# Kernel tuning notes

Hardware: AMD Instinct MI355X
Metric: run time of the kernel (lower is better)

## Reference

```python
import jax, jax.numpy as jnp
import numpy as np

# static config (matches init_kwargs)
B, T, D = 4, 1024, 512
H, G = 8, 2
HD = D // H            # 64
REP = H // G           # 4
CHUNK = 64
LC = 2 * CHUNK         # left_context = context_chunk_number * chunk_size = 128
MAXPOS = CHUNK + LC    # 192
NLAYER = 4
EPS = 1e-4
NEG = -50000.0


def _ln(x, w, b):
    m = x.mean(-1, keepdims=True)
    v = ((x - m) ** 2).mean(-1, keepdims=True)
    return (x - m) / jnp.sqrt(v + EPS) * w + b


def _chunk_mask(mask_length):
    # get_mask_vector(CHUNK, mask_length, LC)
    corr = (mask_length + CHUNK - 1) // CHUNK * CHUNK
    row = jnp.arange(corr)[:, None]
    col = jnp.arange(corr + LC)[None, :]
    start = (row // CHUNK) * CHUNK
    cm = (col >= start) & (col < start + CHUNK + LC)
    cm = cm[:mask_length, LC:LC + mask_length]
    return jnp.where(cm, 0.0, -jnp.inf)


def _cut_masks(mask, lens):
    # _cut_masks_with_len_vector
    Lm = mask.shape[0]
    lim = (lens + LC)[:, None]                      # [B,1]
    inb = jnp.arange(Lm)[None, :] < lim             # [B,Lm]
    valid = inb[:, :, None] & inb[:, None, :]       # [B,Lm,Lm]
    return jnp.where(valid, mask[None], NEG)


def _attn(xp, wq, wk, wv, wo, rel_tab, mask):
    # GQASelfAttentionRelPos forward. xp:[B,Tp,D], mask:[B,Tp,Tp]
    Bb, Tp, _ = xp.shape
    scale = 1.0 / jnp.sqrt(jnp.float32(HD))
    q = (xp @ wq.T).reshape(Bb, Tp, H, HD) * scale
    k = jnp.repeat((xp @ wk.T).reshape(Bb, Tp, G, HD), REP, axis=2)
    v = jnp.repeat((xp @ wv.T).reshape(Bb, Tp, G, HD), REP, axis=2)
    scores = jnp.einsum('bqhd,bkhd->bhqk', q, k)
    r = jnp.arange(Tp)
    dist = jnp.clip(r[None, :] - r[:, None], -(MAXPOS - 1), MAXPOS - 1) + MAXPOS - 1
    rel = rel_tab[dist]                              # [Tp,Tp,HD], row=query
    scores = scores + jnp.einsum('bqhd,kqd->bhqk', q, rel)  # matches 'bhd,thd->bht'
    scores = scores + mask[:, None]                  # broadcast over heads
    p = jax.nn.softmax(scores, axis=-1)
    out = jnp.einsum('bhqk,bkhd->bqhd', p, v).reshape(Bb, Tp, D)
    return out @ wo.T


def _conv(x, pw1, dw, pw2):
    # Conformer-style ConvModule(d_model, kernel=9): pointwise->GLU->depthwise->SiLU->pointwise
    h = x @ pw1.T                                   # [B,T,2D]
    a, g = jnp.split(h, 2, axis=-1)
    h = a * jax.nn.sigmoid(g)                       # GLU
    h = jnp.transpose(h, (0, 2, 1))                 # [B,D,T]
    h = jax.lax.conv_general_dilated(h, dw[:, None, :], (1,), [(4, 4)],
                                     dimension_numbers=('NCH', 'OIH', 'NCH'),
                                     feature_group_count=D)
    h = jax.nn.silu(h)
    h = jnp.transpose(h, (0, 2, 1))
    return h @ pw2.T


def _ffn(x, w1, w2):
    # SwiGLUFFN(factor=2)
    h = x @ w1.T
    a, b = jnp.split(h, 2, axis=-1)
    return (jax.nn.silu(a) * b) @ w2.T


def setup_inputs() -> dict:
    key = jax.random.key(0)
    ks = iter(jax.random.split(key, 40))
    s = 0.02
    def rn(shape):
        return jax.random.normal(next(ks), shape, jnp.float32) * s
    L = NLAYER
    return {
        'x': jax.random.normal(next(ks), (B, T, D), jnp.float32),
        'audio_len': jax.random.randint(next(ks), (B,), 1, T + 1),
        'ln1_w': jnp.ones((L, D), jnp.float32), 'ln1_b': jnp.zeros((L, D), jnp.float32),
        'wq': rn((L, D, D)), 'wk': rn((L, G * HD, D)), 'wv': rn((L, G * HD, D)), 'wo': rn((L, D, D)),
        'rel_emb': rn((L, 2 * MAXPOS - 1, HD)),
        'ln2_w': jnp.ones((L, D), jnp.float32), 'ln2_b': jnp.zeros((L, D), jnp.float32),
        'conv_pw1': rn((L, 2 * D, D)), 'conv_dw': rn((L, D, 9)), 'conv_pw2': rn((L, D, D)),
        'ln3_w': jnp.ones((L, D), jnp.float32), 'ln3_b': jnp.zeros((L, D), jnp.float32),
        'ffn_w1': rn((L, 4 * D, D)), 'ffn_w2': rn((L, D, 2 * D)),
    }


def reference(x, audio_len, ln1_w, ln1_b, wq, wk, wv, wo, rel_emb,
              ln2_w, ln2_b, conv_pw1, conv_dw, conv_pw2,
              ln3_w, ln3_b, ffn_w1, ffn_w2):
    mask = _cut_masks(_chunk_mask(T + LC), audio_len)   # [B,Tp,Tp]
    for i in range(NLAYER):
        x = _ln(x, ln1_w[i], ln1_b[i])
        xp = jnp.pad(x, ((0, 0), (LC, 0), (0, 0)))
        x = x + _attn(xp, wq[i], wk[i], wv[i], wo[i], rel_emb[i], mask)[:, LC:]
        x = _ln(x, ln2_w[i], ln2_b[i])
        x = x + _conv(x, conv_pw1[i], conv_dw[i], conv_pw2[i])
        x = _ln(x, ln3_w[i], ln3_b[i])
        x = x + _ffn(x, ffn_w1[i], ffn_w2[i])
    return x
```

## Files before the change

kernel.cpp:

```cpp
#include <hip/hip_runtime.h>
#include <hip/hip_bf16.h>

typedef __hip_bfloat16 bf16;
typedef unsigned short ushort_t;
typedef unsigned int uint_t;
typedef __attribute__((ext_vector_type(8))) short short8;
typedef __attribute__((ext_vector_type(4))) float floatx4;

__device__ __forceinline__ float b2f(bf16 x) { return __bfloat162float(x); }
__device__ __forceinline__ ushort_t f2us(float f) { bf16 h = __float2bfloat16(f); return *(ushort_t*)&h; }
__device__ __forceinline__ float us2f(ushort_t u) { return __uint_as_float(((uint_t)u) << 16); }

constexpr int Bc = 4, Tc = 1024, Dc = 512, Hc = 8, HDc = 64;
constexpr int LCc = 128, MPc = 192;
constexpr float EPSc = 1e-4f;
constexpr int NBT = Bc * Tc;
constexpr long NE = (long)NBT * Dc;
constexpr float NEGB = -1e30f;
constexpr int PSTRIDE = 8704;
constexpr int QSTR = 768;

__device__ __forceinline__ float wload(const void* p, long i, int f32) {
  return f32 ? ((const float*)p)[i] : b2f(((const bf16*)p)[i]);
}

template<int N> __device__ __forceinline__ void vmwait() {
  if constexpr (N == 0)      asm volatile("s_waitcnt vmcnt(0)" ::: "memory");
  else if constexpr (N == 4) asm volatile("s_waitcnt vmcnt(4)" ::: "memory");
  else if constexpr (N == 6) asm volatile("s_waitcnt vmcnt(6)" ::: "memory");
  else if constexpr (N == 8) asm volatile("s_waitcnt vmcnt(8)" ::: "memory");
  else if constexpr (N == 12) asm volatile("s_waitcnt vmcnt(12)" ::: "memory");
  else static_assert(N == 0, "unsupported vmcnt literal");
}

__device__ __forceinline__ void stage_swz(const ushort_t* __restrict__ G, int rowStride,
                                          int rowBase, int k0, ushort_t* L, int nChunk, int t) {
#pragma unroll
  for (int i = t; i < nChunk; i += 256) {
    int r = i >> 3;
    int cs = (i & 7) ^ (r & 7);
    const ushort_t* gp = G + (long)(rowBase + r) * rowStride + k0 + cs * 8;
    __builtin_amdgcn_global_load_lds(
        (const __attribute__((address_space(1))) void*)gp,
        (__attribute__((address_space(3))) void*)&L[(i & ~63) * 8], 16, 0, 0);
  }
}

__global__ void k_detect(const void* __restrict__ x, int* __restrict__ flag) {
  __shared__ int s[256];
  int t = threadIdx.x;
  const unsigned short* u = (const unsigned short*)x;
  int bad = 0;
  for (int j = t; j < 2048; j += 256) {
    int e = (u[j] >> 7) & 0xFF;
    if (e == 0xFF || e > 0x8F || (e != 0 && e < 0x6F)) bad++;
  }
  s[t] = bad;
  __syncthreads();
  for (int off = 128; off > 0; off >>= 1) { if (t < off) s[t] += s[t + off]; __syncthreads(); }
  if (t == 0) flag[0] = (s[0] > 16) ? 1 : 0;
}

__global__ void k_in(const void* __restrict__ in, float* __restrict__ out, int n,
                     const int* __restrict__ flag) {
  int i = blockIdx.x * 256 + threadIdx.x;
  if (i < n) out[i] = wload(in, i, flag[0]);
}
__global__ void k_out(const float* __restrict__ in, void* __restrict__ out, int n,
                      const int* __restrict__ flag) {
  int i = blockIdx.x * 256 + threadIdx.x;
  if (i >= n) return;
  if (flag[0]) ((float*)out)[i] = in[i];
  else         ((bf16*)out)[i] = __float2bfloat16(in[i]);
}

__global__ void k_w2all(const void* wq, const void* wk, const void* wv, const void* wo,
                        const void* rel, const void* pw1, const void* dwv, const void* pw2,
                        const void* w1, const void* w2,
                        ushort_t* __restrict__ wbf, const int* __restrict__ flag) {
  int f32 = flag[0];
  long i = (long)blockIdx.x * 256 + threadIdx.x;
  if (i >= 12175104L) return;
  float v;
  if (i < 1572864) {
    long l = i / 393216, rem = i - l * 393216;
    int r = (int)(rem >> 9), c = (int)(rem & 511);
    if (r < 512)      v = 0.125f * wload(wq, l * 262144 + (long)r * 512 + c, f32);
    else if (r < 640) v = wload(wk, l * 65536 + (long)(r - 512) * 512 + c, f32);
    else              v = wload(wv, l * 65536 + (long)(r - 640) * 512 + c, f32);
  } else if (i < 2621440) {
    v = wload(wo, i - 1572864, f32);
  } else if (i < 2719488) {
    v = wload(rel, i - 2621440, f32);
  } else if (i < 4816640) {
    v = wload(pw1, i - 2719488, f32);
  } else if (i < 4835072) {
    long r2 = i - 4816640;
    long l = r2 / 4608, rem = r2 - l * 4608;
    int j = (int)(rem >> 9), d = (int)(rem & 511);
    v = wload(dwv, l * 4608 + (long)d * 9 + j, f32);
  } else if (i < 5883648) {
    v = wload(pw2, i - 4835072, f32);
  } else if (i < 10077952) {
    v = wload(w1, i - 5883648, f32);
  } else {
    v = wload(w2, i - 10077952, f32);
  }
  wbf[i] = f2us(v);
}

__global__ __launch_bounds__(256) void k_ln(const float* __restrict__ x,
    const void* __restrict__ w, const void* __restrict__ bb, long woff,
    float* __restrict__ o, ushort_t* __restrict__ oA, const int* __restrict__ flag) {
  int f32 = flag[0];
  int row = blockIdx.x;
  int t = threadIdx.x;
  int lane = t & 63, wv = t >> 6;
  float2 v = ((const float2*)(x + (long)row * Dc))[t];
  float s = v.x + v.y;
#pragma unroll
  for (int o2 = 1; o2 < 64; o2 <<= 1) s += __shfl_xor(s, o2, 64);
  __shared__ float ws[8];
  if (lane == 0) ws[wv] = s;
  __syncthreads();
  float mean = (ws[0] + ws[1] + ws[2] + ws[3]) * (1.0f / Dc);
  float dx = v.x - mean, dy = v.y - mean;
  float s2 = dx * dx + dy * dy;
#pragma unroll
  for (int o2 = 1; o2 < 64; o2 <<= 1) s2 += __shfl_xor(s2, o2, 64);
  if (lane == 0) ws[4 + wv] = s2;
  __syncthreads();
  float inv = 1.0f / sqrtf((ws[4] + ws[5] + ws[6] + ws[7]) * (1.0f / Dc) + EPSc);
  float v0 = dx * inv * wload(w, woff + 2 * t, f32)     + wload(bb, woff + 2 * t, f32);
  float v1 = dy * inv * wload(w, woff + 2 * t + 1, f32) + wload(bb, woff + 2 * t + 1, f32);
  float2 ov; ov.x = v0; ov.y = v1;
  ((float2*)(o + (long)row * Dc))[t] = ov;
  ((uint_t*)(oA + (long)row * Dc))[t] = (uint_t)f2us(v0) | ((uint_t)f2us(v1) << 16);
}

template<int BM, int BN, bool OBF>
__global__ __launch_bounds__(256) void k_gemm_b(const ushort_t* __restrict__ A, int lda,
    const ushort_t* __restrict__ W, void* __restrict__ C, int ldc,
    const float* __restrict__ addend, float alpha, int K) {
  constexpr int WGM = BM / 64;
  constexpr int WGN = 4 / WGM;
  constexpr int WN = BN / WGN;
  constexpr int NJ = WN / 16;
  constexpr int LPI = (BM * 8 + BN * 8) / 256;
  __shared__ ushort_t As[2][BM * 64];
  __shared__ ushort_t Ws[2][BN * 64];
  int t = threadIdx.x;
  int m0 = blockIdx.y * BM, n0 = blockIdx.x * BN;
  int lane = t & 63, wv = t >> 6;
  int l15 = lane & 15, quad = lane >> 4;
  int wrow = (WGM == 2) ? (wv >> 1) * 64 : 0;
  int wcol = (WGM == 2) ? (wv & 1) * WN : wv * WN;
  floatx4 acc[4][NJ];
#pragma unroll
  for (int i = 0; i < 4; ++i)
#pragma unroll
    for (int j = 0; j < NJ; ++j) acc[i][j] = 0;
  stage_swz(A, lda, m0, 0, As[0], BM * 8, t);
  stage_swz(W, K,  n0, 0, Ws[0], BN * 8, t);
  int cur = 0;
  for (int k0 = 0; k0 < K; k0 += 64) {
    int nk = k0 + 64;
    if (nk < K) {
      stage_swz(A, lda, m0, nk, As[cur ^ 1], BM * 8, t);
      stage_swz(W, K,  n0, nk, Ws[cur ^ 1], BN * 8, t);
      vmwait<LPI>();
    } else {
      vmwait<0>();
    }
    __builtin_amdgcn_s_barrier();
    __builtin_amdgcn_sched_barrier(0);
    const ushort_t* Asc = As[cur];
    const ushort_t* Wsc = Ws[cur];
#pragma unroll
    for (int half = 0; half < 2; ++half) {
      int sw = ((half * 4 + quad) ^ (l15 & 7)) << 3;
      short8 af[4], bfr[NJ];
#pragma unroll
      for (int i = 0; i < 4; ++i) af[i] = *(short8*)&Asc[(wrow + i * 16 + l15) * 64 + sw];
#pragma unroll
      for (int j = 0; j < NJ; ++j) bfr[j] = *(short8*)&Wsc[(wcol + j * 16 + l15) * 64 + sw];
#pragma unroll
      for (int i = 0; i < 4; ++i)
#pragma unroll
        for (int j = 0; j < NJ; ++j)
          acc[i][j] = __builtin_amdgcn_mfma_f32_16x16x32_bf16(af[i], bfr[j], acc[i][j], 0, 0, 0);
    }
    __builtin_amdgcn_s_barrier();
    cur ^= 1;
  }
#pragma unroll
  for (int i = 0; i < 4; ++i) {
#pragma unroll
    for (int j = 0; j < NJ; ++j) {
#pragma unroll
      for (int rg = 0; rg < 4; ++rg) {
        int m = m0 + wrow + i * 16 + quad * 4 + rg;
        int n = n0 + wcol + j * 16 + l15;
        float v = alpha * acc[i][j][rg];
        if (addend) v += addend[(long)m * ldc + n];
        if (OBF) ((ushort_t*)C)[(long)m * ldc + n] = f2us(v);
        else     ((float*)C)[(long)m * ldc + n] = v;
      }
    }
  }
}

template<int MODE>
__global__ __launch_bounds__(256) void k_gemm_gate(const ushort_t* __restrict__ A, int lda,
    const ushort_t* __restrict__ Wa, const ushort_t* __restrict__ Wg,
    ushort_t* __restrict__ C, int ldc, int K) {
  __shared__ ushort_t As[2][64 * 64];
  __shared__ ushort_t Wsa[2][64 * 64];
  __shared__ ushort_t Wsg[2][64 * 64];
  int t = threadIdx.x;
  int m0 = blockIdx.y * 64, n0 = blockIdx.x * 64;
  int lane = t & 63, wv = t >> 6;
  int l15 = lane & 15, quad = lane >> 4;
  int wcol = wv * 16;
  floatx4 acca[4], accg[4];
#pragma unroll
  for (int i = 0; i < 4; ++i) { acca[i] = 0; accg[i] = 0; }
  stage_swz(A, lda, m0, 0, As[0], 512, t);
  stage_swz(Wa, K, n0, 0, Wsa[0], 512, t);
  stage_swz(Wg, K, n0, 0, Wsg[0], 512, t);
  int cur = 0;
  for (int k0 = 0; k0 < K; k0 += 64) {
    int nk = k0 + 64;
    if (nk < K) {
      stage_swz(A, lda, m0, nk, As[cur ^ 1], 512, t);
      stage_swz(Wa, K, n0, nk, Wsa[cur ^ 1], 512, t);
      stage_swz(Wg, K, n0, nk, Wsg[cur ^ 1], 512, t);
      vmwait<6>();
    } else {
      vmwait<0>();
    }
    __builtin_amdgcn_s_barrier();
    __builtin_amdgcn_sched_barrier(0);
    const ushort_t* Asc = As[cur];
    const ushort_t* Wac = Wsa[cur];
    const ushort_t* Wgc = Wsg[cur];
#pragma unroll
    for (int half = 0; half < 2; ++half) {
      int sw = ((half * 4 + quad) ^ (l15 & 7)) << 3;
      short8 af[4], ba, bg;
#pragma unroll
      for (int i = 0; i < 4; ++i) af[i] = *(short8*)&Asc[(i * 16 + l15) * 64 + sw];
      ba = *(short8*)&Wac[(wcol + l15) * 64 + sw];
      bg = *(short8*)&Wgc[(wcol + l15) * 64 + sw];
#pragma unroll
      for (int i = 0; i < 4; ++i) {
        acca[i] = __builtin_amdgcn_mfma_f32_16x16x32_bf16(af[i], ba, acca[i], 0, 0, 0);
        accg[i] = __builtin_amdgcn_mfma_f32_16x16x32_bf16(af[i], bg, accg[i], 0, 0, 0);
      }
    }
    __builtin_amdgcn_s_barrier();
    cur ^= 1;
  }
#pragma unroll
  for (int i = 0; i < 4; ++i) {
#pragma unroll
    for (int rg = 0; rg < 4; ++rg) {
      int m = m0 + i * 16 + quad * 4 + rg;
      int n = n0 + wcol + l15;
      float a = acca[i][rg], g = accg[i][rg];
      float v;
      if (MODE == 0) v = a * (1.0f / (1.0f + __expf(-g)));
      else           v = (a / (1.0f + __expf(-a))) * g;
      C[(long)m * ldc + n] = f2us(v);
    }
  }
}

__global__ __launch_bounds__(256, 3) void k_attn(const ushort_t* __restrict__ qkv,
    const ushort_t* __restrict__ relL, const int* __restrict__ alen,
    ushort_t* __restrict__ out, char* __restrict__ part) {
  int bx = blockIdx.x;
  int h = blockIdx.y, b = blockIdx.z;
  int len = alen[b];
  int inv, qt, grp;
  if (bx < 16) { inv = 0; qt = bx; grp = 0; }
  else         { inv = 1; qt = (bx - 16) & 15; grp = (bx - 16) >> 4; }
  int q0 = qt * 64;
  if (inv) { if (q0 + 64 <= len) return; }
  else     { if (q0 >= len) return; }
  int nvalid = min(len - q0, 64);
  int g = h >> 2;
  __shared__ __align__(16) ushort_t UQB[8704];
  __shared__ __align__(16) ushort_t Ks[64 * 64];
  __shared__ __align__(16) ushort_t Vt[64 * 72];
  __shared__ __align__(16) ushort_t Ps[64 * 64];
  __shared__ __align__(16) float fML[128];
  ushort_t* Qs = UQB;
  ushort_t* B2t = UQB;
  int t = threadIdx.x;
  int lane = t & 63, w = t >> 6;
  int l15 = lane & 15, quad = lane >> 4;
  int qw = w * 16;
  {
    int qi = t >> 2, du = (t & 3) * 16;
    const ushort_t* src = qkv + ((long)(b * Tc + q0 + qi)) * QSTR + h * 64 + du;
    *(uint4*)&Qs[qi * 72 + du] = *(const uint4*)(src);
    *(uint4*)&Qs[qi * 72 + du + 8] = *(const uint4*)(src + 8);
  }
  const int koB = inv ? -128 : (q0 - 128);
  const int KSTEP = inv ? 4 : 1;
  const int nIt = inv ? ((grp < 2) ? 5 : 4) : 3;
  uint4 kr0, kr1, vr0, vr1;
  int kj = t >> 2, du = (t & 3) * 16, c0 = du >> 3;
  auto LOADKV = [&](int kt2) {
    int ko = koB + kt2 * 64 + kj;
    if (ko >= 0) {
      long basek = ((long)(b * Tc + ko)) * QSTR + 512 + g * 64 + du;
      kr0 = *(const uint4*)(qkv + basek);
      kr1 = *(const uint4*)(qkv + basek + 8);
      vr0 = *(const uint4*)(qkv + basek + 128);
      vr1 = *(const uint4*)(qkv + basek + 136);
    } else {
      uint4 z = {0, 0, 0, 0};
      kr0 = z; kr1 = z; vr0 = z; vr1 = z;
    }
  };
  LOADKV(grp);
  float m_ = NEGB, l_ = 0.f;
  floatx4 acc[4];
#pragma unroll
  for (int j = 0; j < 4; ++j) acc[j] = 0;
  __syncthreads();
  short8 aq0 = *(short8*)&Qs[(qw + l15) * 72 + quad * 8];
  short8 aq1 = *(short8*)&Qs[(qw + l15) * 72 + 32 + quad * 8];
  float rv_lo = 0.f, rv_hi = 0.f;
  if (inv) {
    int er = (l15 == 1) ? 382 : 0;
    short8 be0 = *(const short8*)(relL + (long)er * 64 + quad * 8);
    short8 be1 = *(const short8*)(relL + (long)er * 64 + 32 + quad * 8);
    floatx4 ec = {0.f, 0.f, 0.f, 0.f};
    ec = __builtin_amdgcn_mfma_f32_16x16x32_bf16(be0, aq0, ec, 0, 0, 0);
    ec = __builtin_amdgcn_mfma_f32_16x16x32_bf16(be1, aq1, ec, 0, 0, 0);
    rv_lo = __shfl(ec[0], l15, 64);
    rv_hi = __shfl(ec[1], l15, 64);
  }
  int sw7 = l15 & 7;
  for (int it = 0; it < nIt; ++it) {
    int kt = inv ? (grp + it * KSTEP) : it;
    int ko0 = koB + kt * 64;
    int t0 = q0 - ko0 + 191;
    bool far_hi = (q0 - ko0 - 63) >= 191;
    bool far_lo = (q0 + 63 - ko0) <= -191;
    bool near = !far_hi && !far_lo;
    int cb = min(max(t0 - 63, 0), 255);
    __syncthreads();
    {
      *(uint4*)&Ks[kj * 64 + ((c0 ^ (kj & 7)) << 3)] = kr0;
      *(uint4*)&Ks[kj * 64 + (((c0 + 1) ^ (kj & 7)) << 3)] = kr1;
      uint_t wds[8] = {vr0.x, vr0.y, vr0.z, vr0.w, vr1.x, vr1.y, vr1.z, vr1.w};
#pragma unroll
      for (int u = 0; u < 8; ++u) {
        Vt[(du + 2 * u) * 72 + kj] = (ushort_t)(wds[u] & 0xffff);
        Vt[(du + 2 * u + 1) * 72 + kj] = (ushort_t)(wds[u] >> 16);
      }
    }
    if (near) {
      __builtin_amdgcn_s_setprio(1);
#pragma unroll
      for (int p = 0; p < 2; ++p) {
        short8 rw0[4], rw1[4];
#pragma unroll
        for (int j = 0; j < 4; ++j) {
          long wr = cb + (p * 4 + j) * 16 + l15;
          rw0[j] = *(const short8*)(relL + wr * 64 + quad * 8);
          rw1[j] = *(const short8*)(relL + wr * 64 + 32 + quad * 8);
        }
#pragma unroll
        for (int j = 0; j < 4; ++j) {
          floatx4 z = {0.f, 0.f, 0.f, 0.f};
          z = __builtin_amdgcn_mfma_f32_16x16x32_bf16(rw0[j], aq0, z, 0, 0, 0);
          z = __builtin_amdgcn_mfma_f32_16x16x32_bf16(rw1[j], aq1, z, 0, 0, 0);
#pragma unroll
          for (int rg = 0; rg < 4; ++rg) {
            int cpr = (p * 4 + j) * 16 + quad * 4 + rg;
            B2t[cpr * 68 + qw + l15] = f2us(z[rg]);
          }
        }
      }
      __builtin_amdgcn_s_setprio(0);
    }
    __syncthreads();
    if (it + 1 < nIt) LOADKV(kt + KSTEP);
    floatx4 s[4];
    __builtin_amdgcn_s_setprio(1);
#pragma unroll
    for (int nt = 0; nt < 4; ++nt) {
      short8 ak0 = *(short8*)&Ks[(nt * 16 + l15) * 64 + ((quad ^ sw7) << 3)];
      short8 ak1 = *(short8*)&Ks[(nt * 16 + l15) * 64 + (((4 + quad) ^ sw7) << 3)];
      floatx4 z = {0.f, 0.f, 0.f, 0.f};
      z = __builtin_amdgcn_mfma_f32_16x16x32_bf16(ak0, aq0, z, 0, 0, 0);
      z = __builtin_amdgcn_mfma_f32_16x16x32_bf16(ak1, aq1, z, 0, 0, 0);
      s[nt] = z;
    }
    __builtin_amdgcn_s_setprio(0);
    if (near) {
#pragma unroll
      for (int nt = 0; nt < 4; ++nt)
#pragma unroll
        for (int rg = 0; rg < 4; ++rg) {
          int c = t0 + qw + l15 - (nt * 16 + quad * 4 + rg);
          c = min(max(c, 0), 382);
          s[nt][rg] += us2f(B2t[(c - cb) * 68 + qw + l15]);
        }
    } else {
      float rv = far_hi ? rv_hi : rv_lo;
#pragma unroll
      for (int nt = 0; nt < 4; ++nt)
#pragma unroll
        for (int rg = 0; rg < 4; ++rg) s[nt][rg] += rv;
    }
    if (!inv) {
#pragma unroll
      for (int nt = 0; nt < 4; ++nt)
#pragma unroll
        for (int rg = 0; rg < 4; ++rg) {
          int ko = ko0 + nt * 16 + quad * 4 + rg;
          if (ko >= len) s[nt][rg] = NEGB;
        }
    }
    float mx = s[0][0];
#pragma unroll
    for (int nt = 0; nt < 4; ++nt)
#pragma unroll
      for (int rg = 0; rg < 4; ++rg) mx = fmaxf(mx, s[nt][rg]);
    mx = fmaxf(mx, __shfl_xor(mx, 16, 64));
    mx = fmaxf(mx, __shfl_xor(mx, 32, 64));
    float mn = fmaxf(m_, mx);
    float al = __expf(m_ - mn);
    float ps = 0.f;
#pragma unroll
    for (int nt = 0; nt < 4; ++nt)
#pragma unroll
      for (int rg = 0; rg < 4; ++rg) {
        float p = __expf(s[nt][rg] - mn);
        s[nt][rg] = p;
        ps += p;
      }
    ps += __shfl_xor(ps, 16, 64);
    ps += __shfl_xor(ps, 32, 64);
    l_ = l_ * al + ps;
    m_ = mn;
    if (quad == 0) fML[qw + l15] = al;
#pragma unroll
    for (int nt = 0; nt < 4; ++nt)
#pragma unroll
      for (int pr = 0; pr < 2; ++pr) {
        uint_t pk = (uint_t)f2us(s[nt][2 * pr]) | ((uint_t)f2us(s[nt][2 * pr + 1]) << 16);
        int e = nt * 16 + quad * 4 + pr * 2;
        *(uint_t*)&Ps[(qw + l15) * 64 + (((e >> 3) ^ sw7) << 3) + (e & 7)] = pk;
      }
    floatx4 av = *(floatx4*)&fML[qw + quad * 4];
#pragma unroll
    for (int j = 0; j < 4; ++j)
#pragma unroll
      for (int rg = 0; rg < 4; ++rg) acc[j][rg] *= av[rg];
    short8 ap0 = *(short8*)&Ps[(qw + l15) * 64 + ((quad ^ sw7) << 3)];
    short8 ap1 = *(short8*)&Ps[(qw + l15) * 64 + (((4 + quad) ^ sw7) << 3)];
    __builtin_amdgcn_s_setprio(1);
#pragma unroll
    for (int j = 0; j < 4; ++j) {
      short8 bv0 = *(short8*)&Vt[(j * 16 + l15) * 72 + quad * 8];
      short8 bv1 = *(short8*)&Vt[(j * 16 + l15) * 72 + 32 + quad * 8];
      acc[j] = __builtin_amdgcn_mfma_f32_16x16x32_bf16(ap0, bv0, acc[j], 0, 0, 0);
      acc[j] = __builtin_amdgcn_mfma_f32_16x16x32_bf16(ap1, bv1, acc[j], 0, 0, 0);
    }
    __builtin_amdgcn_s_setprio(0);
  }
  if (inv) {
    char* pp = part + (long)((((b * 8 + h) * 16 + qt) * 4 + grp)) * PSTRIDE;
    ushort_t* Cp = (ushort_t*)pp;
    float* mp = (float*)(pp + 8192);
#pragma unroll
    for (int j = 0; j < 4; ++j)
#pragma unroll
      for (int rg = 0; rg < 4; ++rg)
        Cp[(qw + quad * 4 + rg) * 64 + j * 16 + l15] = f2us(acc[j][rg]);
    if (quad == 0) { mp[qw + l15] = m_; mp[64 + qw + l15] = l_; }
  } else {
    if (quad == 0) fML[64 + qw + l15] = l_;
    floatx4 lv = *(floatx4*)&fML[64 + qw + quad * 4];
#pragma unroll
    for (int rg = 0; rg < 4; ++rg) {
      int R = qw + quad * 4 + rg;
      if (R < nvalid) {
        float invL = 1.0f / lv[rg];
#pragma unroll
        for (int j = 0; j < 4; ++j)
          out[((long)(b * Tc + q0 + R)) * Dc + h * 64 + j * 16 + l15] = f2us(acc[j][rg] * invL);
      }
    }
  }
}

__global__ __launch_bounds__(256) void k_comb(const char* __restrict__ part,
    const int* __restrict__ alen, ushort_t* __restrict__ out) {
  int qt = blockIdx.x, h = blockIdx.y, b = blockIdx.z;
  int len = alen[b];
  int q0 = qt * 64;
  if (q0 + 64 <= len) return;
  int nskip = max(len - q0, 0);
  int t = threadIdx.x;
  int d = t & 63, r0 = (t >> 6) * 16;
  const char* pb = part + (long)(((b * 8 + h) * 16 + qt) * 4) * PSTRIDE;
#pragma unroll 4
  for (int i = 0; i < 16; ++i) {
    int r = r0 + i;
    if (r < nskip) continue;
    float mg[4], lg[4], M = NEGB;
#pragma unroll
    for (int g2 = 0; g2 < 4; ++g2) {
      const float* mp = (const float*)(pb + g2 * PSTRIDE + 8192);
      mg[g2] = mp[r];
      lg[g2] = mp[64 + r];
      M = fmaxf(M, mg[g2]);
    }
    float L = 0.f, wgt[4];
#pragma unroll
    for (int g2 = 0; g2 < 4; ++g2) { wgt[g2] = __expf(mg[g2] - M); L += lg[g2] * wgt[g2]; }
    float v = 0.f;
#pragma unroll
    for (int g2 = 0; g2 < 4; ++g2)
      v += us2f(((const ushort_t*)(pb + g2 * PSTRIDE))[r * 64 + d]) * wgt[g2];
    out[((long)(b * Tc + q0 + r)) * Dc + h * 64 + d] = f2us(v / L);
  }
}

__global__ void k_dwconv(const ushort_t* __restrict__ in, const ushort_t* __restrict__ dwT,
                         ushort_t* __restrict__ out, int n8) {
  int i = blockIdx.x * 256 + threadIdx.x;
  if (i >= n8) return;
  int row = i >> 6;
  int d8 = (i & 63) << 3;
  int t = row & (Tc - 1);
  int b = row >> 10;
  float acc[8] = {0, 0, 0, 0, 0, 0, 0, 0};
#pragma unroll
  for (int j = 0; j < 9; ++j) {
    int tt = t + j - 4;
    if (tt < 0 || tt >= Tc) continue;
    short8 vv = *(const short8*)&in[((long)(b * Tc + tt) << 9) + d8];
    short8 dv = *(const short8*)&dwT[j * 512 + d8];
#pragma unroll
    for (int e = 0; e < 8; ++e)
      acc[e] += us2f((ushort_t)vv[e]) * us2f((ushort_t)dv[e]);
  }
  short8 o8;
#pragma unroll
  for (int e = 0; e < 8; ++e)
    o8[e] = (short)f2us(acc[e] * (1.0f / (1.0f + __expf(-acc[e]))));
  *(short8*)&out[(long)row * 512 + d8] = o8;
}

extern "C" void kernel_launch(void* const* d_in, const int* in_sizes, int n_in,
                              void* d_out, int out_size, void* d_ws, size_t ws_size,
                              hipStream_t stream) {
  const void* x_in = d_in[0];
  const int*  alen = (const int*)d_in[1];
  const void* ln1w = d_in[2];
  const void* ln1b = d_in[3];
  const void* wq   = d_in[4];
  const void* wk   = d_in[5];
  const void* wv   = d_in[6];
  const void* wo   = d_in[7];
  const void* rel  = d_in[8];
  const void* ln2w = d_in[9];
  const void* ln2b = d_in[10];
  const void* pw1  = d_in[11];
  const void* dwv  = d_in[12];
  const void* pw2  = d_in[13];
  const void* ln3w = d_in[14];
  const void* ln3b = d_in[15];
  const void* w1   = d_in[16];
  const void* w2   = d_in[17];

  char* base = (char*)d_ws;
  int*      flag = (int*)base;
  float*    xf   = (float*)(base + 256);
  float*    lnb  = (float*)(base + 256 + 8388608);
  ushort_t* lnA  = (ushort_t*)(base + 16777472);
  ushort_t* wbf  = (ushort_t*)(base + 20971776);
  char*     U    = base + 45321984;
  ushort_t* qkv = (ushort_t*)U;
  ushort_t* ab  = (ushort_t*)(U + 6291456);
  char*     partA = U + 10485760;
  ushort_t* big = (ushort_t*)U;
  ushort_t* cb  = (ushort_t*)(U + 16777216);
  size_t REQ = 45321984 + 16777216 + 4194304;
  size_t REQ2 = 45321984 + 35651584;
  if (REQ2 > REQ) REQ = REQ2;
  if (ws_size < REQ) return;

  ushort_t* qkvB  = wbf + 0;
  ushort_t* woB   = wbf + 1572864;
  ushort_t* relB  = wbf + 2621440;
  ushort_t* pw1B  = wbf + 2719488;
  ushort_t* dwB   = wbf + 4816640;
  ushort_t* pw2B  = wbf + 4835072;
  ushort_t* w1B   = wbf + 5883648;
  ushort_t* w2B   = wbf + 10077952;

  k_detect<<<1, 256, 0, stream>>>(x_in, flag);
  k_in<<<(int)((NE + 255) / 256), 256, 0, stream>>>(x_in, xf, (int)NE, flag);
  k_w2all<<<47559, 256, 0, stream>>>(wq, wk, wv, wo, rel, pw1, dwv, pw2, w1, w2, wbf, flag);

  for (int i = 0; i < 4; ++i) {
    long oLN = (long)i * Dc;
    k_ln<<<NBT, 256, 0, stream>>>(xf, ln1w, ln1b, oLN, lnb, lnA, flag);
    k_gemm_b<64, 64, true><<<dim3(12, 64), 256, 0, stream>>>(lnA, Dc, qkvB + (long)i * 393216, qkv, QSTR, nullptr, 1.0f, 512);
    k_attn<<<dim3(80, 8, 4), 256, 0, stream>>>(qkv, relB + (long)i * 24512, alen, ab, partA);
    k_comb<<<dim3(16, 8, 4), 256, 0, stream>>>(partA, alen, ab);
    k_gemm_b<64, 64, false><<<dim3(8, 64), 256, 0, stream>>>(ab, Dc, woB + (long)i * 262144, xf, Dc, lnb, 1.0f, 512);

    k_ln<<<NBT, 256, 0, stream>>>(xf, ln2w, ln2b, oLN, lnb, lnA, flag);
    k_gemm_gate<0><<<dim3(8, 64), 256, 0, stream>>>(lnA, Dc, pw1B + (long)i * 524288,
        pw1B + (long)i * 524288 + 262144, big, 512, 512);
    k_dwconv<<<NBT * 512 / 8 / 256, 256, 0, stream>>>(big, dwB + (long)i * 4608, cb, NBT * 512 / 8);
    k_gemm_b<64, 64, false><<<dim3(8, 64), 256, 0, stream>>>(cb, Dc, pw2B + (long)i * 262144, xf, Dc, lnb, 1.0f, 512);

    k_ln<<<NBT, 256, 0, stream>>>(xf, ln3w, ln3b, oLN, lnb, lnA, flag);
    k_gemm_gate<1><<<dim3(16, 64), 256, 0, stream>>>(lnA, Dc, w1B + (long)i * 1048576,
        w1B + (long)i * 1048576 + 524288, big, 1024, 512);
    k_gemm_b<64, 64, false><<<dim3(8, 64), 256, 0, stream>>>(big, 1024, w2B + (long)i * 524288, xf, Dc, lnb, 1.0f, 1024);
  }

  k_out<<<(int)((NE + 255) / 256), 256, 0, stream>>>(xf, d_out, (int)NE, flag);
}
```

Before: 833.4 us.

## Write V transposed from QKV GEMM, load Q into registers, warp-per-row LayerNorm

```diff
diff --git a/kernel.cpp b/kernel.cpp
--- a/kernel.cpp
+++ b/kernel.cpp
@@ -29,7 +29,6 @@
   else if constexpr (N == 4) asm volatile("s_waitcnt vmcnt(4)" ::: "memory");
   else if constexpr (N == 6) asm volatile("s_waitcnt vmcnt(6)" ::: "memory");
   else if constexpr (N == 8) asm volatile("s_waitcnt vmcnt(8)" ::: "memory");
-  else if constexpr (N == 12) asm volatile("s_waitcnt vmcnt(12)" ::: "memory");
   else static_assert(N == 0, "unsupported vmcnt literal");
 }
 
@@ -113,35 +112,42 @@
     const void* __restrict__ w, const void* __restrict__ bb, long woff,
     float* __restrict__ o, ushort_t* __restrict__ oA, const int* __restrict__ flag) {
   int f32 = flag[0];
-  int row = blockIdx.x;
   int t = threadIdx.x;
-  int lane = t & 63, wv = t >> 6;
-  float2 v = ((const float2*)(x + (long)row * Dc))[t];
-  float s = v.x + v.y;
+  int lane = t & 63;
+  int row = blockIdx.x * 4 + (t >> 6);
+  const float4* xr = (const float4*)(x + (long)row * Dc);
+  float4 va = xr[lane * 2], vb = xr[lane * 2 + 1];
+  float s = va.x + va.y + va.z + va.w + vb.x + vb.y + vb.z + vb.w;
 #pragma unroll
   for (int o2 = 1; o2 < 64; o2 <<= 1) s += __shfl_xor(s, o2, 64);
-  __shared__ float ws[8];
-  if (lane == 0) ws[wv] = s;
-  __syncthreads();
-  float mean = (ws[0] + ws[1] + ws[2] + ws[3]) * (1.0f / Dc);
-  float dx = v.x - mean, dy = v.y - mean;
-  float s2 = dx * dx + dy * dy;
+  float mean = s * (1.0f / Dc);
+  float d[8] = {va.x - mean, va.y - mean, va.z - mean, va.w - mean,
+                vb.x - mean, vb.y - mean, vb.z - mean, vb.w - mean};
+  float s2 = 0.f;
+#pragma unroll
+  for (int e = 0; e < 8; ++e) s2 += d[e] * d[e];
 #pragma unroll
   for (int o2 = 1; o2 < 64; o2 <<= 1) s2 += __shfl_xor(s2, o2, 64);
-  if (lane == 0) ws[4 + wv] = s2;
-  __syncthreads();
-  float inv = 1.0f / sqrtf((ws[4] + ws[5] + ws[6] + ws[7]) * (1.0f / Dc) + EPSc);
-  float v0 = dx * inv * wload(w, woff + 2 * t, f32)     + wload(bb, woff + 2 * t, f32);
-  float v1 = dy * inv * wload(w, woff + 2 * t + 1, f32) + wload(bb, woff + 2 * t + 1, f32);
-  float2 ov; ov.x = v0; ov.y = v1;
-  ((float2*)(o + (long)row * Dc))[t] = ov;
-  ((uint_t*)(oA + (long)row * Dc))[t] = (uint_t)f2us(v0) | ((uint_t)f2us(v1) << 16);
-}
-
-template<int BM, int BN, bool OBF>
+  float inv = 1.0f / sqrtf(s2 * (1.0f / Dc) + EPSc);
+  float v[8];
+#pragma unroll
+  for (int e = 0; e < 8; ++e)
+    v[e] = d[e] * inv * wload(w, woff + lane * 8 + e, f32) + wload(bb, woff + lane * 8 + e, f32);
+  float4 o0 = {v[0], v[1], v[2], v[3]}, o1 = {v[4], v[5], v[6], v[7]};
+  float4* orow = (float4*)(o + (long)row * Dc);
+  orow[lane * 2] = o0; orow[lane * 2 + 1] = o1;
+  uint4 pk;
+  pk.x = (uint_t)f2us(v[0]) | ((uint_t)f2us(v[1]) << 16);
+  pk.y = (uint_t)f2us(v[2]) | ((uint_t)f2us(v[3]) << 16);
+  pk.z = (uint_t)f2us(v[4]) | ((uint_t)f2us(v[5]) << 16);
+  pk.w = (uint_t)f2us(v[6]) | ((uint_t)f2us(v[7]) << 16);
+  *(uint4*)&oA[(long)row * Dc + lane * 8] = pk;
+}
+
+template<int BM, int BN, bool OBF, int QKV>
 __global__ __launch_bounds__(256) void k_gemm_b(const ushort_t* __restrict__ A, int lda,
     const ushort_t* __restrict__ W, void* __restrict__ C, int ldc,
-    const float* __restrict__ addend, float alpha, int K) {
+    const float* __restrict__ addend, float alpha, int K, ushort_t* __restrict__ vtw) {
   constexpr int WGM = BM / 64;
   constexpr int WGN = 4 / WGM;
   constexpr int WN = BN / WGN;
@@ -193,6 +199,18 @@
     __builtin_amdgcn_s_barrier();
     cur ^= 1;
   }
+  if (QKV && n0 >= 640) {
+#pragma unroll
+    for (int i = 0; i < 4; ++i) {
+      int mb = m0 + i * 16 + quad * 4;
+      int d = n0 - 640 + wcol + l15;
+      uint2 pk;
+      pk.x = (uint_t)f2us(acc[i][0][0]) | ((uint_t)f2us(acc[i][0][1]) << 16);
+      pk.y = (uint_t)f2us(acc[i][0][2]) | ((uint_t)f2us(acc[i][0][3]) << 16);
+      *(uint2*)(vtw + ((long)(mb >> 10)) * 131072 + (long)d * 1024 + (mb & 1023)) = pk;
+    }
+    return;
+  }
 #pragma unroll
   for (int i = 0; i < 4; ++i) {
 #pragma unroll
@@ -277,6 +295,7 @@
 }
 
 __global__ __launch_bounds__(256, 3) void k_attn(const ushort_t* __restrict__ qkv,
+    const ushort_t* __restrict__ vt,
     const ushort_t* __restrict__ relL, const int* __restrict__ alen,
     ushort_t* __restrict__ out, char* __restrict__ part) {
   int bx = blockIdx.x;
@@ -290,36 +309,33 @@
   else     { if (q0 >= len) return; }
   int nvalid = min(len - q0, 64);
   int g = h >> 2;
-  __shared__ __align__(16) ushort_t UQB[8704];
+  __shared__ __align__(16) ushort_t B2t[8704];
   __shared__ __align__(16) ushort_t Ks[64 * 64];
-  __shared__ __align__(16) ushort_t Vt[64 * 72];
+  __shared__ __align__(16) ushort_t Vt[64 * 64];
   __shared__ __align__(16) ushort_t Ps[64 * 64];
   __shared__ __align__(16) float fML[128];
-  ushort_t* Qs = UQB;
-  ushort_t* B2t = UQB;
   int t = threadIdx.x;
   int lane = t & 63, w = t >> 6;
   int l15 = lane & 15, quad = lane >> 4;
   int qw = w * 16;
-  {
-    int qi = t >> 2, du = (t & 3) * 16;
-    const ushort_t* src = qkv + ((long)(b * Tc + q0 + qi)) * QSTR + h * 64 + du;
-    *(uint4*)&Qs[qi * 72 + du] = *(const uint4*)(src);
-    *(uint4*)&Qs[qi * 72 + du + 8] = *(const uint4*)(src + 8);
-  }
+  const ushort_t* qrow = qkv + ((long)(b * Tc + q0 + qw + l15)) * QSTR + h * 64;
+  short8 aq0 = *(const short8*)(qrow + quad * 8);
+  short8 aq1 = *(const short8*)(qrow + 32 + quad * 8);
   const int koB = inv ? -128 : (q0 - 128);
   const int KSTEP = inv ? 4 : 1;
   const int nIt = inv ? ((grp < 2) ? 5 : 4) : 3;
   uint4 kr0, kr1, vr0, vr1;
   int kj = t >> 2, du = (t & 3) * 16, c0 = du >> 3;
+  int vd = t >> 2, vc = (t & 3) * 2;
   auto LOADKV = [&](int kt2) {
-    int ko = koB + kt2 * 64 + kj;
-    if (ko >= 0) {
-      long basek = ((long)(b * Tc + ko)) * QSTR + 512 + g * 64 + du;
+    int ko0x = koB + kt2 * 64;
+    if (ko0x >= 0) {
+      long basek = ((long)(b * Tc + ko0x + kj)) * QSTR + 512 + g * 64 + du;
       kr0 = *(const uint4*)(qkv + basek);
       kr1 = *(const uint4*)(qkv + basek + 8);
-      vr0 = *(const uint4*)(qkv + basek + 128);
-      vr1 = *(const uint4*)(qkv + basek + 136);
+      long basev = (long)b * 131072 + (long)(g * 64 + vd) * 1024 + ko0x + (t & 3) * 16;
+      vr0 = *(const uint4*)(vt + basev);
+      vr1 = *(const uint4*)(vt + basev + 8);
     } else {
       uint4 z = {0, 0, 0, 0};
       kr0 = z; kr1 = z; vr0 = z; vr1 = z;
@@ -330,9 +346,6 @@
   floatx4 acc[4];
 #pragma unroll
   for (int j = 0; j < 4; ++j) acc[j] = 0;
-  __syncthreads();
-  short8 aq0 = *(short8*)&Qs[(qw + l15) * 72 + quad * 8];
-  short8 aq1 = *(short8*)&Qs[(qw + l15) * 72 + 32 + quad * 8];
   float rv_lo = 0.f, rv_hi = 0.f;
   if (inv) {
     int er = (l15 == 1) ? 382 : 0;
@@ -357,12 +370,8 @@
     {
       *(uint4*)&Ks[kj * 64 + ((c0 ^ (kj & 7)) << 3)] = kr0;
       *(uint4*)&Ks[kj * 64 + (((c0 + 1) ^ (kj & 7)) << 3)] = kr1;
-      uint_t wds[8] = {vr0.x, vr0.y, vr0.z, vr0.w, vr1.x, vr1.y, vr1.z, vr1.w};
-#pragma unroll
-      for (int u = 0; u < 8; ++u) {
-        Vt[(du + 2 * u) * 72 + kj] = (ushort_t)(wds[u] & 0xffff);
-        Vt[(du + 2 * u + 1) * 72 + kj] = (ushort_t)(wds[u] >> 16);
-      }
+      *(uint4*)&Vt[vd * 64 + ((vc ^ (vd & 7)) << 3)] = vr0;
+      *(uint4*)&Vt[vd * 64 + (((vc + 1) ^ (vd & 7)) << 3)] = vr1;
     }
     if (near) {
       __builtin_amdgcn_s_setprio(1);
@@ -469,8 +478,9 @@
     __builtin_amdgcn_s_setprio(1);
 #pragma unroll
     for (int j = 0; j < 4; ++j) {
-      short8 bv0 = *(short8*)&Vt[(j * 16 + l15) * 72 + quad * 8];
-      short8 bv1 = *(short8*)&Vt[(j * 16 + l15) * 72 + 32 + quad * 8];
+      int rd = j * 16 + l15;
+      short8 bv0 = *(short8*)&Vt[rd * 64 + ((quad ^ (rd & 7)) << 3)];
+      short8 bv1 = *(short8*)&Vt[rd * 64 + (((4 + quad) ^ (rd & 7)) << 3)];
       acc[j] = __builtin_amdgcn_mfma_f32_16x16x32_bf16(ap0, bv0, acc[j], 0, 0, 0);
       acc[j] = __builtin_amdgcn_mfma_f32_16x16x32_bf16(ap1, bv1, acc[j], 0, 0, 0);
     }
@@ -488,6 +498,7 @@
     if (quad == 0) { mp[qw + l15] = m_; mp[64 + qw + l15] = l_; }
   } else {
     if (quad == 0) fML[64 + qw + l15] = l_;
+    __syncthreads();
     floatx4 lv = *(floatx4*)&fML[64 + qw + quad * 4];
 #pragma unroll
     for (int rg = 0; rg < 4; ++rg) {
@@ -592,7 +603,8 @@
   char*     U    = base + 45321984;
   ushort_t* qkv = (ushort_t*)U;
   ushort_t* ab  = (ushort_t*)(U + 6291456);
-  char*     partA = U + 10485760;
+  ushort_t* vtb = (ushort_t*)(U + 10485760);
+  char*     partA = U + 11534336;
   ushort_t* big = (ushort_t*)U;
   ushort_t* cb  = (ushort_t*)(U + 16777216);
   size_t REQ = 45321984 + 16777216 + 4194304;
@@ -615,22 +627,22 @@
 
   for (int i = 0; i < 4; ++i) {
     long oLN = (long)i * Dc;
-    k_ln<<<NBT, 256, 0, stream>>>(xf, ln1w, ln1b, oLN, lnb, lnA, flag);
-    k_gemm_b<64, 64, true><<<dim3(12, 64), 256, 0, stream>>>(lnA, Dc, qkvB + (long)i * 393216, qkv, QSTR, nullptr, 1.0f, 512);
-    k_attn<<<dim3(80, 8, 4), 256, 0, stream>>>(qkv, relB + (long)i * 24512, alen, ab, partA);
+    k_ln<<<NBT / 4, 256, 0, stream>>>(xf, ln1w, ln1b, oLN, lnb, lnA, flag);
+    k_gemm_b<64, 64, true, 1><<<dim3(12, 64), 256, 0, stream>>>(lnA, Dc, qkvB + (long)i * 393216, qkv, QSTR, nullptr, 1.0f, 512, vtb);
+    k_attn<<<dim3(80, 8, 4), 256, 0, stream>>>(qkv, vtb, relB + (long)i * 24512, alen, ab, partA);
     k_comb<<<dim3(16, 8, 4), 256, 0, stream>>>(partA, alen, ab);
-    k_gemm_b<64, 64, false><<<dim3(8, 64), 256, 0, stream>>>(ab, Dc, woB + (long)i * 262144, xf, Dc, lnb, 1.0f, 512);
-
-    k_ln<<<NBT, 256, 0, stream>>>(xf, ln2w, ln2b, oLN, lnb, lnA, flag);
+    k_gemm_b<64, 64, false, 0><<<dim3(8, 64), 256, 0, stream>>>(ab, Dc, woB + (long)i * 262144, xf, Dc, lnb, 1.0f, 512, nullptr);
+
+    k_ln<<<NBT / 4, 256, 0, stream>>>(xf, ln2w, ln2b, oLN, lnb, lnA, flag);
     k_gemm_gate<0><<<dim3(8, 64), 256, 0, stream>>>(lnA, Dc, pw1B + (long)i * 524288,
         pw1B + (long)i * 524288 + 262144, big, 512, 512);
     k_dwconv<<<NBT * 512 / 8 / 256, 256, 0, stream>>>(big, dwB + (long)i * 4608, cb, NBT * 512 / 8);
-    k_gemm_b<64, 64, false><<<dim3(8, 64), 256, 0, stream>>>(cb, Dc, pw2B + (long)i * 262144, xf, Dc, lnb, 1.0f, 512);
-
-    k_ln<<<NBT, 256, 0, stream>>>(xf, ln3w, ln3b, oLN, lnb, lnA, flag);
+    k_gemm_b<64, 64, false, 0><<<dim3(8, 64), 256, 0, stream>>>(cb, Dc, pw2B + (long)i * 262144, xf, Dc, lnb, 1.0f, 512, nullptr);
+
+    k_ln<<<NBT / 4, 256, 0, stream>>>(xf, ln3w, ln3b, oLN, lnb, lnA, flag);
     k_gemm_gate<1><<<dim3(16, 64), 256, 0, stream>>>(lnA, Dc, w1B + (long)i * 1048576,
         w1B + (long)i * 1048576 + 524288, big, 1024, 512);
-    k_gemm_b<64, 64, false><<<dim3(8, 64), 256, 0, stream>>>(big, 1024, w2B + (long)i * 524288, xf, Dc, lnb, 1.0f, 1024);
+    k_gemm_b<64, 64, false, 0><<<dim3(8, 64), 256, 0, stream>>>(big, 1024, w2B + (long)i * 524288, xf, Dc, lnb, 1.0f, 1024, nullptr);
   }
 
   k_out<<<(int)((NE + 255) / 256), 256, 0, stream>>>(xf, d_out, (int)NE, flag);
```

Result: slower. 873.3 us (+4.8%).
